# Kernel optimization log

Hardware: AMD Instinct MI355X
Metric: run time of the kernel (lower is better)

## Reference

```python
import jax, jax.numpy as jnp
import numpy as np

N_NODES = 50000


def _gcn_norm(edge_index, num_nodes):
    # PyG gcn_norm with add_self_loops=True, edge_weight=1
    loops = jnp.arange(num_nodes, dtype=edge_index.dtype)
    src = jnp.concatenate([edge_index[0], loops])
    dst = jnp.concatenate([edge_index[1], loops])
    deg = jax.ops.segment_sum(jnp.ones_like(dst, dtype=jnp.float32), dst,
                              num_segments=num_nodes)
    deg_inv_sqrt = jnp.where(deg > 0, jax.lax.rsqrt(jnp.maximum(deg, 1.0)), 0.0)
    norm = deg_inv_sqrt[src] * deg_inv_sqrt[dst]  # [E + N]
    return src, dst, norm


def _gcn_conv(x, src, dst, norm, W, b, num_nodes):
    h = x @ W                                 # [N, out] dense transform first
    msg = h[src] * norm[:, None]              # gather + scale, [E+N, out]
    out = jax.ops.segment_sum(msg, dst, num_segments=num_nodes)  # scatter-add
    return out + b


def setup_inputs() -> dict:
    key = jax.random.key(0)
    k1, k2, k3, k4, k5 = jax.random.split(key, 5)
    in_ch, out_ch = 128, 64
    hid = 2 * out_ch
    x = jax.random.normal(k1, (N_NODES, in_ch), dtype=jnp.float32)
    edge_index = jax.random.randint(k2, (2, 800000), 0, N_NODES, dtype=jnp.int64)
    # Glorot init like PyG GCNConv
    W1 = jax.random.normal(k3, (in_ch, hid), dtype=jnp.float32) * (1.0 / np.sqrt(in_ch))
    b1 = jnp.zeros((hid,), dtype=jnp.float32)
    W2 = jax.random.normal(k4, (hid, out_ch), dtype=jnp.float32) * (1.0 / np.sqrt(hid))
    b2 = jnp.zeros((out_ch,), dtype=jnp.float32)
    return {"x": x, "edge_index": edge_index, "W1": W1, "b1": b1,
            "W2": W2, "b2": b2}


def reference(x, edge_index, W1, b1, W2, b2):
    num_nodes = x.shape[0]
    src, dst, norm = _gcn_norm(edge_index, num_nodes)
    h = _gcn_conv(x, src, dst, norm, W1, b1, num_nodes)
    h = jax.nn.relu(h)
    return _gcn_conv(h, src, dst, norm, W2, b2, num_nodes)
```

## Files before the change

### kernel.cpp

```cpp
#include <hip/hip_runtime.h>

#define N_NODES 50000
#define N_EDGES 800000
#define IN_CH   128
#define HID     128
#define OUT_CH  64

#define NBUCK 196
#define BCAP  5120
#define XPAD  136

#define G1_BLOCKS ((N_NODES + 63) / 64)
#define GSPLIT 391

typedef __attribute__((ext_vector_type(8))) short bf16x8;
typedef __attribute__((ext_vector_type(4))) float f32x4;
typedef unsigned short ushort_t;

__device__ __forceinline__ unsigned short f2bf(float f) {
    unsigned u = __float_as_uint(f);
    u += 0x7fffu + ((u >> 16) & 1u);
    return (unsigned short)(u >> 16);
}
__device__ __forceinline__ unsigned pack2(float a, float b) {
    return (unsigned)f2bf(a) | ((unsigned)f2bf(b) << 16);
}
__device__ __forceinline__ float bf_lo(unsigned u) { return __uint_as_float(u << 16); }
__device__ __forceinline__ float bf_hi(unsigned u) { return __uint_as_float(u & 0xffff0000u); }


__global__ __launch_bounds__(256) void k_prep(const float* __restrict__ W1,
                                              const float* __restrict__ W2,
                                              ushort_t* __restrict__ W1t,
                                              ushort_t* __restrict__ W2t,
                                              int* __restrict__ bcur) {
    if (blockIdx.x == 0 && threadIdx.x < NBUCK) bcur[threadIdx.x] = 0;
    int i = blockIdx.x * 256 + threadIdx.x;
    if (i < 128 * 128) {
        int k = i >> 7, c = i & 127;
        W1t[c * 128 + k] = f2bf(W1[k * 128 + c]);
    } else {
        int j = i - 128 * 128;
        if (j < 128 * 64) {
            int k = j >> 6, c = j & 63;
            W2t[c * 128 + k] = f2bf(W2[k * 64 + c]);
        }
    }
}


__global__ __launch_bounds__(256) void k_stage(const int phase, const int tile0,
                                               const int* __restrict__ src,
                                               const int* __restrict__ dst,
                                               int* __restrict__ bcur,
                                               unsigned* __restrict__ rec,
                                               const float* __restrict__ x,
                                               const ushort_t* __restrict__ W1t,
                                               ushort_t* __restrict__ g,
                                               int* __restrict__ row_beg,
                                               int* __restrict__ row_end,
                                               float* __restrict__ dis,
                                               int* __restrict__ col) {
    __shared__ char smem[52224];
    const int tid = threadIdx.x;

    if (blockIdx.x < NBUCK) {
        if (phase == 0) {
            int* cnt  = (int*)smem;
            int* boff = cnt + 256;
            int* gdel = boff + 256;
            int* bid  = gdel + 256;
            unsigned* stage = (unsigned*)(bid + 4096);

            const int base = blockIdx.x * 4096;
            const int nval = min(4096, N_EDGES - base);

            int dreg[16];
#pragma unroll
            for (int k = 0; k < 16; ++k) {
                int e = base + k * 256 + tid;
                dreg[k] = (e < N_EDGES) ? dst[e] : -1;
            }
            cnt[tid] = 0;
            __syncthreads();
#pragma unroll
            for (int k = 0; k < 16; ++k)
                if (dreg[k] >= 0) atomicAdd(&cnt[dreg[k] >> 8], 1);
            __syncthreads();
            int* s = bid;
            int c = cnt[tid];
            s[tid] = c;
            __syncthreads();
            for (int off = 1; off < 256; off <<= 1) {
                int u = (tid >= off) ? s[tid - off] : 0;
                __syncthreads();
                s[tid] += u;
                __syncthreads();
            }
            boff[tid] = s[tid] - c;
            if (tid < NBUCK && c > 0)
                gdel[tid] = tid * BCAP + atomicAdd(&bcur[tid], c) - boff[tid];
            __syncthreads();
            cnt[tid] = 0;
            __syncthreads();
#pragma unroll
            for (int k = 0; k < 16; ++k) {
                int e = base + k * 256 + tid;
                if (dreg[k] >= 0) {
                    int b = dreg[k] >> 8;
                    int rk = atomicAdd(&cnt[b], 1);
                    int p = boff[b] + rk;
                    stage[p] = (unsigned)src[e] | ((unsigned)(dreg[k] & 255) << 16);
                    bid[p] = b;
                }
            }
            __syncthreads();
            for (int i = tid; i < nval; i += 256) {
                int b = bid[i];
                int p = i + gdel[b];
                if (p < (b + 1) * BCAP)
                    rec[p] = stage[i];
            }
        } else {
            int* hist = (int*)smem;
            int* sbuf = hist + 256;
            int* cur  = sbuf + 256;
            unsigned* stage = (unsigned*)(cur + 256);
            const int b = blockIdx.x;
            const int lo = b * BCAP;
            const int cnt = min(bcur[b], BCAP);

            hist[tid] = 0;
            __syncthreads();
            for (int j = tid; j < cnt; j += 256)
                atomicAdd(&hist[rec[lo + j] >> 16], 1);
            __syncthreads();
            int deg = hist[tid];
            sbuf[tid] = deg;
            __syncthreads();
            for (int off = 1; off < 256; off <<= 1) {
                int u = (tid >= off) ? sbuf[tid - off] : 0;
                __syncthreads();
                sbuf[tid] += u;
                __syncthreads();
            }
            int lbeg = sbuf[tid] - deg;
            int node = (b << 8) + tid;
            if (node < N_NODES) {
                row_beg[node] = lo + lbeg;
                row_end[node] = lo + lbeg + deg;
                dis[node] = rsqrtf((float)deg + 1.0f);
            }
            cur[tid] = lbeg;
            __syncthreads();
            for (int j = tid; j < cnt; j += 256) {
                unsigned r = rec[lo + j];
                int rk = atomicAdd(&cur[r >> 16], 1);
                stage[rk] = r & 0xffffu;
            }
            __syncthreads();
            for (int i = tid; i < cnt; i += 256)
                col[lo + i] = (int)stage[i];
        }
    } else {
        ushort_t* xs = (ushort_t*)smem;
        ushort_t* ws = (ushort_t*)(smem + 17408);
        const int bid = tile0 + (blockIdx.x - NBUCK);
        const int row0 = bid * 64;

        for (int i = tid; i < 64 * 32; i += 256) {
            int r = i >> 5, k4 = (i & 31) << 2;
            int gr = row0 + r;
            float4 v = make_float4(0.f, 0.f, 0.f, 0.f);
            if (gr < N_NODES) v = *(const float4*)&x[(long)gr * IN_CH + k4];
            ushort4 u;
            u.x = f2bf(v.x); u.y = f2bf(v.y); u.z = f2bf(v.z); u.w = f2bf(v.w);
            *(ushort4*)&xs[r * XPAD + k4] = u;
        }
        for (int i = tid; i < 128 * 16; i += 256) {
            int c = i >> 4, seg = i & 15;
            *(uint4*)&ws[c * XPAD + seg * 8] = *(const uint4*)&W1t[c * 128 + seg * 8];
        }
        __syncthreads();

        const int w = tid >> 6, lane = tid & 63;
        const int m = lane & 15, q = lane >> 4;
        const ushort_t* arow = &xs[(w * 16 + m) * XPAD + q * 8];
        const ushort_t* brow = &ws[m * XPAD + q * 8];

        f32x4 acc[8] = {};
#pragma unroll
        for (int k0 = 0; k0 < 128; k0 += 32) {
            bf16x8 a = *(const bf16x8*)(arow + k0);
#pragma unroll
            for (int nt = 0; nt < 8; ++nt) {
                bf16x8 b = *(const bf16x8*)(brow + nt * 16 * XPAD + k0);
                acc[nt] = __builtin_amdgcn_mfma_f32_16x16x32_bf16(a, b, acc[nt], 0, 0, 0);
            }
        }

#pragma unroll
        for (int reg = 0; reg < 4; ++reg) {
            int gr = row0 + w * 16 + q * 4 + reg;
            if (gr < N_NODES) {
#pragma unroll
                for (int nt = 0; nt < 8; ++nt)
                    g[(long)gr * HID + nt * 16 + m] = f2bf(acc[nt][reg]);
            }
        }
    }
}


__global__ __launch_bounds__(256) void k_agg1g2(const int* __restrict__ row_beg,
                                                const int* __restrict__ row_end,
                                                const int* __restrict__ col,
                                                const float* __restrict__ dis,
                                                const ushort_t* __restrict__ g1,
                                                const float* __restrict__ b1,
                                                const ushort_t* __restrict__ W2t,
                                                ushort_t* __restrict__ g3) {
    __shared__ ushort_t hs[16 * XPAD];
    const int tid = threadIdx.x;
    const int w = tid >> 6, lane = tid & 63;
    const int q = lane >> 4;
    const int seg = lane & 15;
    const int cl = seg << 3;
    const uint4* G = (const uint4*)g1;
    const int r0 = blockIdx.x * 16;

    for (int rr = 0; rr < 4; ++rr) {
        const int r = r0 + w * 4 + rr;
        const int beg = row_beg[r], end = row_end[r];

        float acc[8] = {};
        int e = beg + q;
        for (; e + 4 < end; e += 8) {
            int s0 = col[e], s1 = col[e + 4];
            float d0 = dis[s0], d1 = dis[s1];
            uint4 u0 = G[(long)s0 * 16 + seg];
            uint4 u1 = G[(long)s1 * 16 + seg];
            acc[0] += bf_lo(u0.x) * d0; acc[1] += bf_hi(u0.x) * d0;
            acc[2] += bf_lo(u0.y) * d0; acc[3] += bf_hi(u0.y) * d0;
            acc[4] += bf_lo(u0.z) * d0; acc[5] += bf_hi(u0.z) * d0;
            acc[6] += bf_lo(u0.w) * d0; acc[7] += bf_hi(u0.w) * d0;
            acc[0] += bf_lo(u1.x) * d1; acc[1] += bf_hi(u1.x) * d1;
            acc[2] += bf_lo(u1.y) * d1; acc[3] += bf_hi(u1.y) * d1;
            acc[4] += bf_lo(u1.z) * d1; acc[5] += bf_hi(u1.z) * d1;
            acc[6] += bf_lo(u1.w) * d1; acc[7] += bf_hi(u1.w) * d1;
        }
        if (e < end) {
            int s0 = col[e];
            float d0 = dis[s0];
            uint4 u = G[(long)s0 * 16 + seg];
            acc[0] += bf_lo(u.x) * d0; acc[1] += bf_hi(u.x) * d0;
            acc[2] += bf_lo(u.y) * d0; acc[3] += bf_hi(u.y) * d0;
            acc[4] += bf_lo(u.z) * d0; acc[5] += bf_hi(u.z) * d0;
            acc[6] += bf_lo(u.w) * d0; acc[7] += bf_hi(u.w) * d0;
        }
#pragma unroll
        for (int off = 16; off < 64; off <<= 1)
#pragma unroll
            for (int j = 0; j < 8; ++j) acc[j] += __shfl_xor(acc[j], off);

        if (q == 0) {
            const float d = dis[r];
            uint4 u = G[(long)r * 16 + seg];
            acc[0] += bf_lo(u.x) * d; acc[1] += bf_hi(u.x) * d;
            acc[2] += bf_lo(u.y) * d; acc[3] += bf_hi(u.y) * d;
            acc[4] += bf_lo(u.z) * d; acc[5] += bf_hi(u.z) * d;
            acc[6] += bf_lo(u.w) * d; acc[7] += bf_hi(u.w) * d;
            float o[8];
#pragma unroll
            for (int j = 0; j < 8; ++j) o[j] = fmaxf(acc[j] * d + b1[cl + j], 0.f);
            uint4 pw;
            pw.x = pack2(o[0], o[1]); pw.y = pack2(o[2], o[3]);
            pw.z = pack2(o[4], o[5]); pw.w = pack2(o[6], o[7]);
            *(uint4*)&hs[(w * 4 + rr) * XPAD + cl] = pw;
        }
    }
    __syncthreads();

    const int m = lane & 15;
    const ushort_t* arow = &hs[m * XPAD + q * 8];
    const ushort_t* brow = &W2t[(w * 16 + m) * 128 + q * 8];

    f32x4 acc2 = {};
#pragma unroll
    for (int k0 = 0; k0 < 128; k0 += 32) {
        bf16x8 a = *(const bf16x8*)(arow + k0);
        bf16x8 b = *(const bf16x8*)(brow + k0);
        acc2 = __builtin_amdgcn_mfma_f32_16x16x32_bf16(a, b, acc2, 0, 0, 0);
    }

#pragma unroll
    for (int reg = 0; reg < 4; ++reg) {
        int gr = r0 + q * 4 + reg;
        float d = dis[gr];
        g3[(long)gr * OUT_CH + w * 16 + m] = f2bf(acc2[reg] * d);
    }
}


__global__ __launch_bounds__(256) void k_agg2(const int* __restrict__ row_beg,
                                              const int* __restrict__ row_end,
                                              const int* __restrict__ col,
                                              const float* __restrict__ dis,
                                              const ushort_t* __restrict__ g3,
                                              const float* __restrict__ b2,
                                              float* __restrict__ out) {
    int r = blockIdx.x * 4 + (threadIdx.x >> 6);
    if (r >= N_NODES) return;
    const int lane = threadIdx.x & 63;
    const int q = lane >> 3;
    const int seg = lane & 7;
    const int cl = seg << 3;
    const uint4* G = (const uint4*)g3;
    const int beg = row_beg[r], end = row_end[r];

    float acc[8] = {};
    int e = beg + q;
    for (; e + 8 < end; e += 16) {
        int s0 = col[e], s1 = col[e + 8];
        uint4 u0 = G[(long)s0 * 8 + seg];
        uint4 u1 = G[(long)s1 * 8 + seg];
        acc[0] += bf_lo(u0.x); acc[1] += bf_hi(u0.x);
        acc[2] += bf_lo(u0.y); acc[3] += bf_hi(u0.y);
        acc[4] += bf_lo(u0.z); acc[5] += bf_hi(u0.z);
        acc[6] += bf_lo(u0.w); acc[7] += bf_hi(u0.w);
        acc[0] += bf_lo(u1.x); acc[1] += bf_hi(u1.x);
        acc[2] += bf_lo(u1.y); acc[3] += bf_hi(u1.y);
        acc[4] += bf_lo(u1.z); acc[5] += bf_hi(u1.z);
        acc[6] += bf_lo(u1.w); acc[7] += bf_hi(u1.w);
    }
    if (e < end) {
        int s = col[e];
        uint4 u = G[(long)s * 8 + seg];
        acc[0] += bf_lo(u.x); acc[1] += bf_hi(u.x);
        acc[2] += bf_lo(u.y); acc[3] += bf_hi(u.y);
        acc[4] += bf_lo(u.z); acc[5] += bf_hi(u.z);
        acc[6] += bf_lo(u.w); acc[7] += bf_hi(u.w);
    }
#pragma unroll
    for (int off = 8; off < 64; off <<= 1)
#pragma unroll
        for (int j = 0; j < 8; ++j) acc[j] += __shfl_xor(acc[j], off);

    if (q == 0) {
        uint4 u = G[(long)r * 8 + seg];
        acc[0] += bf_lo(u.x); acc[1] += bf_hi(u.x);
        acc[2] += bf_lo(u.y); acc[3] += bf_hi(u.y);
        acc[4] += bf_lo(u.z); acc[5] += bf_hi(u.z);
        acc[6] += bf_lo(u.w); acc[7] += bf_hi(u.w);
        const float d = dis[r];
        float4 o0, o1;
        o0.x = acc[0] * d + b2[cl + 0];
        o0.y = acc[1] * d + b2[cl + 1];
        o0.z = acc[2] * d + b2[cl + 2];
        o0.w = acc[3] * d + b2[cl + 3];
        o1.x = acc[4] * d + b2[cl + 4];
        o1.y = acc[5] * d + b2[cl + 5];
        o1.z = acc[6] * d + b2[cl + 6];
        o1.w = acc[7] * d + b2[cl + 7];
        *(float4*)&out[(long)r * OUT_CH + cl] = o0;
        *(float4*)&out[(long)r * OUT_CH + cl + 4] = o1;
    }
}


extern "C" void kernel_launch(void* const* d_in, const int* in_sizes, int n_in,
                              void* d_out, int out_size, void* d_ws, size_t ws_size,
                              hipStream_t stream) {
    const float* x   = (const float*)d_in[0];
    const int*   ei  = (const int*)d_in[1];
    const float* W1  = (const float*)d_in[2];
    const float* b1  = (const float*)d_in[3];
    const float* W2  = (const float*)d_in[4];
    const float* b2  = (const float*)d_in[5];
    float* out = (float*)d_out;

    const int* src = ei;
    const int* dst = ei + N_EDGES;

    char* p = (char*)d_ws;
    unsigned* rec = (unsigned*)p;         p += (long)NBUCK * BCAP * 4;
    int* col     = (int*)p;               p += (long)NBUCK * BCAP * 4;
    int* row_beg = (int*)p;               p += 50048 * 4;
    int* row_end = (int*)p;               p += 50048 * 4;
    int* bcur    = (int*)p;               p += 256 * 4;
    float* dis   = (float*)p;             p += 50048 * 4;
    ushort_t* W1t = (ushort_t*)p;         p += 128 * 128 * 2;
    ushort_t* W2t = (ushort_t*)p;         p += 128 * 64 * 2;
    ushort_t* g1  = (ushort_t*)p;         p += (long)N_NODES * HID * 2;
    ushort_t* g3  = (ushort_t*)p;

    const int B = 256;

    k_prep<<<96, B, 0, stream>>>(W1, W2, W1t, W2t, bcur);
    k_stage<<<NBUCK + GSPLIT, B, 0, stream>>>(0, 0, src, dst, bcur, rec,
                                              x, W1t, g1, row_beg, row_end, dis, col);
    k_stage<<<NBUCK + (G1_BLOCKS - GSPLIT), B, 0, stream>>>(1, GSPLIT, src, dst, bcur, rec,
                                              x, W1t, g1, row_beg, row_end, dis, col);
    k_agg1g2<<<3125, B, 0, stream>>>(row_beg, row_end, col, dis, g1, b1, W2t, g3);
    k_agg2<<<(N_NODES + 3) / 4, B, 0, stream>>>(row_beg, row_end, col, dis, g3, b2, out);
}
```

Measured before the change: 173.0 us.

## Drop global CSR build; rebuild per-bucket CSR in shared memory inside aggregation kernels

Removes the phase-1 CSR pass that wrote col/row_beg/row_end to global memory. A small k_dis kernel now computes degrees, and each aggregation block re-sorts its 256-node bucket's edge records into shared memory before gathering. All GEMM tiles for g1 now run in a single launch alongside bucketing. This saves global writes and reads of the column index arrays and one launch, but every block repeats the bucket histogram, scan and scatter 16 times per bucket in both aggregation kernels.

```diff
diff --git a/kernel.cpp b/kernel.cpp
--- a/kernel.cpp
+++ b/kernel.cpp
@@ -11,7 +11,6 @@
 #define XPAD  136
 
 #define G1_BLOCKS ((N_NODES + 63) / 64)
-#define GSPLIT 391
 
 typedef __attribute__((ext_vector_type(8))) short bf16x8;
 typedef __attribute__((ext_vector_type(4))) float f32x4;
@@ -49,123 +48,76 @@
 }
 
 
-__global__ __launch_bounds__(256) void k_stage(const int phase, const int tile0,
-                                               const int* __restrict__ src,
-                                               const int* __restrict__ dst,
-                                               int* __restrict__ bcur,
-                                               unsigned* __restrict__ rec,
-                                               const float* __restrict__ x,
-                                               const ushort_t* __restrict__ W1t,
-                                               ushort_t* __restrict__ g,
-                                               int* __restrict__ row_beg,
-                                               int* __restrict__ row_end,
-                                               float* __restrict__ dis,
-                                               int* __restrict__ col) {
+__global__ __launch_bounds__(256) void k_stage0(const int* __restrict__ src,
+                                                const int* __restrict__ dst,
+                                                int* __restrict__ bcur,
+                                                unsigned* __restrict__ rec,
+                                                const float* __restrict__ x,
+                                                const ushort_t* __restrict__ W1t,
+                                                ushort_t* __restrict__ g1) {
     __shared__ char smem[52224];
     const int tid = threadIdx.x;
 
     if (blockIdx.x < NBUCK) {
-        if (phase == 0) {
-            int* cnt  = (int*)smem;
-            int* boff = cnt + 256;
-            int* gdel = boff + 256;
-            int* bid  = gdel + 256;
-            unsigned* stage = (unsigned*)(bid + 4096);
-
-            const int base = blockIdx.x * 4096;
-            const int nval = min(4096, N_EDGES - base);
-
-            int dreg[16];
-#pragma unroll
-            for (int k = 0; k < 16; ++k) {
-                int e = base + k * 256 + tid;
-                dreg[k] = (e < N_EDGES) ? dst[e] : -1;
+        int* cnt  = (int*)smem;
+        int* boff = cnt + 256;
+        int* gdel = boff + 256;
+        int* bid  = gdel + 256;
+        unsigned* stage = (unsigned*)(bid + 4096);
+
+        const int base = blockIdx.x * 4096;
+        const int nval = min(4096, N_EDGES - base);
+
+        int dreg[16];
+#pragma unroll
+        for (int k = 0; k < 16; ++k) {
+            int e = base + k * 256 + tid;
+            dreg[k] = (e < N_EDGES) ? dst[e] : -1;
+        }
+        cnt[tid] = 0;
+        __syncthreads();
+#pragma unroll
+        for (int k = 0; k < 16; ++k)
+            if (dreg[k] >= 0) atomicAdd(&cnt[dreg[k] >> 8], 1);
+        __syncthreads();
+        int* s = bid;
+        int c = cnt[tid];
+        s[tid] = c;
+        __syncthreads();
+        for (int off = 1; off < 256; off <<= 1) {
+            int u = (tid >= off) ? s[tid - off] : 0;
+            __syncthreads();
+            s[tid] += u;
+            __syncthreads();
+        }
+        boff[tid] = s[tid] - c;
+        if (tid < NBUCK && c > 0)
+            gdel[tid] = tid * BCAP + atomicAdd(&bcur[tid], c) - boff[tid];
+        __syncthreads();
+        cnt[tid] = 0;
+        __syncthreads();
+#pragma unroll
+        for (int k = 0; k < 16; ++k) {
+            int e = base + k * 256 + tid;
+            if (dreg[k] >= 0) {
+                int b = dreg[k] >> 8;
+                int rk = atomicAdd(&cnt[b], 1);
+                int p = boff[b] + rk;
+                stage[p] = (unsigned)src[e] | ((unsigned)(dreg[k] & 255) << 16);
+                bid[p] = b;
             }
-            cnt[tid] = 0;
-            __syncthreads();
-#pragma unroll
-            for (int k = 0; k < 16; ++k)
-                if (dreg[k] >= 0) atomicAdd(&cnt[dreg[k] >> 8], 1);
-            __syncthreads();
-            int* s = bid;
-            int c = cnt[tid];
-            s[tid] = c;
-            __syncthreads();
-            for (int off = 1; off < 256; off <<= 1) {
-                int u = (tid >= off) ? s[tid - off] : 0;
-                __syncthreads();
-                s[tid] += u;
-                __syncthreads();
-            }
-            boff[tid] = s[tid] - c;
-            if (tid < NBUCK && c > 0)
-                gdel[tid] = tid * BCAP + atomicAdd(&bcur[tid], c) - boff[tid];
-            __syncthreads();
-            cnt[tid] = 0;
-            __syncthreads();
-#pragma unroll
-            for (int k = 0; k < 16; ++k) {
-                int e = base + k * 256 + tid;
-                if (dreg[k] >= 0) {
-                    int b = dreg[k] >> 8;
-                    int rk = atomicAdd(&cnt[b], 1);
-                    int p = boff[b] + rk;
-                    stage[p] = (unsigned)src[e] | ((unsigned)(dreg[k] & 255) << 16);
-                    bid[p] = b;
-                }
-            }
-            __syncthreads();
-            for (int i = tid; i < nval; i += 256) {
-                int b = bid[i];
-                int p = i + gdel[b];
-                if (p < (b + 1) * BCAP)
-                    rec[p] = stage[i];
-            }
-        } else {
-            int* hist = (int*)smem;
-            int* sbuf = hist + 256;
-            int* cur  = sbuf + 256;
-            unsigned* stage = (unsigned*)(cur + 256);
-            const int b = blockIdx.x;
-            const int lo = b * BCAP;
-            const int cnt = min(bcur[b], BCAP);
-
-            hist[tid] = 0;
-            __syncthreads();
-            for (int j = tid; j < cnt; j += 256)
-                atomicAdd(&hist[rec[lo + j] >> 16], 1);
-            __syncthreads();
-            int deg = hist[tid];
-            sbuf[tid] = deg;
-            __syncthreads();
-            for (int off = 1; off < 256; off <<= 1) {
-                int u = (tid >= off) ? sbuf[tid - off] : 0;
-                __syncthreads();
-                sbuf[tid] += u;
-                __syncthreads();
-            }
-            int lbeg = sbuf[tid] - deg;
-            int node = (b << 8) + tid;
-            if (node < N_NODES) {
-                row_beg[node] = lo + lbeg;
-                row_end[node] = lo + lbeg + deg;
-                dis[node] = rsqrtf((float)deg + 1.0f);
-            }
-            cur[tid] = lbeg;
-            __syncthreads();
-            for (int j = tid; j < cnt; j += 256) {
-                unsigned r = rec[lo + j];
-                int rk = atomicAdd(&cur[r >> 16], 1);
-                stage[rk] = r & 0xffffu;
-            }
-            __syncthreads();
-            for (int i = tid; i < cnt; i += 256)
-                col[lo + i] = (int)stage[i];
+        }
+        __syncthreads();
+        for (int i = tid; i < nval; i += 256) {
+            int b = bid[i];
+            int p = i + gdel[b];
+            if (p < (b + 1) * BCAP)
+                rec[p] = stage[i];
         }
     } else {
         ushort_t* xs = (ushort_t*)smem;
         ushort_t* ws = (ushort_t*)(smem + 17408);
-        const int bid = tile0 + (blockIdx.x - NBUCK);
+        const int bid = blockIdx.x - NBUCK;
         const int row0 = bid * 64;
 
         for (int i = tid; i < 64 * 32; i += 256) {
@@ -205,38 +157,89 @@
             if (gr < N_NODES) {
 #pragma unroll
                 for (int nt = 0; nt < 8; ++nt)
-                    g[(long)gr * HID + nt * 16 + m] = f2bf(acc[nt][reg]);
+                    g1[(long)gr * HID + nt * 16 + m] = f2bf(acc[nt][reg]);
             }
         }
     }
 }
 
 
-__global__ __launch_bounds__(256) void k_agg1g2(const int* __restrict__ row_beg,
-                                                const int* __restrict__ row_end,
-                                                const int* __restrict__ col,
-                                                const float* __restrict__ dis,
-                                                const ushort_t* __restrict__ g1,
-                                                const float* __restrict__ b1,
-                                                const ushort_t* __restrict__ W2t,
-                                                ushort_t* __restrict__ g3) {
+__global__ __launch_bounds__(256) void k_dis(const int* __restrict__ bcur,
+                                             const unsigned* __restrict__ rec,
+                                             float* __restrict__ dis) {
+    __shared__ int hist[256];
+    const int tid = threadIdx.x;
+    const int b = blockIdx.x;
+    const int lo = b * BCAP;
+    const int cnt = min(bcur[b], BCAP);
+    hist[tid] = 0;
+    __syncthreads();
+    for (int j = tid; j < cnt; j += 256)
+        atomicAdd(&hist[rec[lo + j] >> 16], 1);
+    __syncthreads();
+    int node = (b << 8) + tid;
+    if (node < N_NODES) dis[node] = rsqrtf((float)hist[tid] + 1.0f);
+}
+
+
+__global__ __launch_bounds__(256) void k_agg1x(const int* __restrict__ bcur,
+                                               const unsigned* __restrict__ rec,
+                                               const float* __restrict__ dis,
+                                               const ushort_t* __restrict__ g1,
+                                               const float* __restrict__ b1,
+                                               const ushort_t* __restrict__ W2t,
+                                               ushort_t* __restrict__ g3) {
+    __shared__ int deg_s[256];
+    __shared__ int beg_s[256];
+    __shared__ int cur_s[256];
+    __shared__ float disl[256];
+    __shared__ int stage_src[BCAP];
     __shared__ ushort_t hs[16 * XPAD];
     const int tid = threadIdx.x;
+    const int b = blockIdx.x >> 4, sl = blockIdx.x & 15;
+    const int lo = b * BCAP;
+    const int cntb = min(bcur[b], BCAP);
+
+    deg_s[tid] = 0;
+    __syncthreads();
+    for (int j = tid; j < cntb; j += 256)
+        atomicAdd(&deg_s[rec[lo + j] >> 16], 1);
+    __syncthreads();
+    int dg = deg_s[tid];
+    cur_s[tid] = dg;
+    __syncthreads();
+    for (int off = 1; off < 256; off <<= 1) {
+        int u = (tid >= off) ? cur_s[tid - off] : 0;
+        __syncthreads();
+        cur_s[tid] += u;
+        __syncthreads();
+    }
+    beg_s[tid] = cur_s[tid] - dg;
+    disl[tid] = rsqrtf((float)dg + 1.0f);
+    cur_s[tid] = beg_s[tid];
+    __syncthreads();
+    for (int j = tid; j < cntb; j += 256) {
+        unsigned r = rec[lo + j];
+        int rk = atomicAdd(&cur_s[r >> 16], 1);
+        stage_src[rk] = (int)(r & 0xffffu);
+    }
+    __syncthreads();
+
     const int w = tid >> 6, lane = tid & 63;
     const int q = lane >> 4;
     const int seg = lane & 15;
     const int cl = seg << 3;
     const uint4* G = (const uint4*)g1;
-    const int r0 = blockIdx.x * 16;
 
     for (int rr = 0; rr < 4; ++rr) {
-        const int r = r0 + w * 4 + rr;
-        const int beg = row_beg[r], end = row_end[r];
+        const int t = sl * 16 + w * 4 + rr;
+        const int r = (b << 8) + t;
+        const int beg = beg_s[t], end = beg + deg_s[t];
 
         float acc[8] = {};
         int e = beg + q;
         for (; e + 4 < end; e += 8) {
-            int s0 = col[e], s1 = col[e + 4];
+            int s0 = stage_src[e], s1 = stage_src[e + 4];
             float d0 = dis[s0], d1 = dis[s1];
             uint4 u0 = G[(long)s0 * 16 + seg];
             uint4 u1 = G[(long)s1 * 16 + seg];
@@ -250,7 +253,7 @@
             acc[6] += bf_lo(u1.w) * d1; acc[7] += bf_hi(u1.w) * d1;
         }
         if (e < end) {
-            int s0 = col[e];
+            int s0 = stage_src[e];
             float d0 = dis[s0];
             uint4 u = G[(long)s0 * 16 + seg];
             acc[0] += bf_lo(u.x) * d0; acc[1] += bf_hi(u.x) * d0;
@@ -264,19 +267,25 @@
             for (int j = 0; j < 8; ++j) acc[j] += __shfl_xor(acc[j], off);
 
         if (q == 0) {
-            const float d = dis[r];
-            uint4 u = G[(long)r * 16 + seg];
-            acc[0] += bf_lo(u.x) * d; acc[1] += bf_hi(u.x) * d;
-            acc[2] += bf_lo(u.y) * d; acc[3] += bf_hi(u.y) * d;
-            acc[4] += bf_lo(u.z) * d; acc[5] += bf_hi(u.z) * d;
-            acc[6] += bf_lo(u.w) * d; acc[7] += bf_hi(u.w) * d;
-            float o[8];
-#pragma unroll
-            for (int j = 0; j < 8; ++j) o[j] = fmaxf(acc[j] * d + b1[cl + j], 0.f);
-            uint4 pw;
-            pw.x = pack2(o[0], o[1]); pw.y = pack2(o[2], o[3]);
-            pw.z = pack2(o[4], o[5]); pw.w = pack2(o[6], o[7]);
-            *(uint4*)&hs[(w * 4 + rr) * XPAD + cl] = pw;
+            const int hrow = w * 4 + rr;
+            if (r < N_NODES) {
+                const float d = disl[t];
+                uint4 u = G[(long)r * 16 + seg];
+                acc[0] += bf_lo(u.x) * d; acc[1] += bf_hi(u.x) * d;
+                acc[2] += bf_lo(u.y) * d; acc[3] += bf_hi(u.y) * d;
+                acc[4] += bf_lo(u.z) * d; acc[5] += bf_hi(u.z) * d;
+                acc[6] += bf_lo(u.w) * d; acc[7] += bf_hi(u.w) * d;
+                float o[8];
+#pragma unroll
+                for (int j = 0; j < 8; ++j) o[j] = fmaxf(acc[j] * d + b1[cl + j], 0.f);
+                uint4 pw;
+                pw.x = pack2(o[0], o[1]); pw.y = pack2(o[2], o[3]);
+                pw.z = pack2(o[4], o[5]); pw.w = pack2(o[6], o[7]);
+                *(uint4*)&hs[hrow * XPAD + cl] = pw;
+            } else {
+                uint4 z = make_uint4(0u, 0u, 0u, 0u);
+                *(uint4*)&hs[hrow * XPAD + cl] = z;
+            }
         }
     }
     __syncthreads();
@@ -295,75 +304,114 @@
 
 #pragma unroll
     for (int reg = 0; reg < 4; ++reg) {
-        int gr = r0 + q * 4 + reg;
-        float d = dis[gr];
-        g3[(long)gr * OUT_CH + w * 16 + m] = f2bf(acc2[reg] * d);
-    }
-}
-
-
-__global__ __launch_bounds__(256) void k_agg2(const int* __restrict__ row_beg,
-                                              const int* __restrict__ row_end,
-                                              const int* __restrict__ col,
-                                              const float* __restrict__ dis,
-                                              const ushort_t* __restrict__ g3,
-                                              const float* __restrict__ b2,
-                                              float* __restrict__ out) {
-    int r = blockIdx.x * 4 + (threadIdx.x >> 6);
-    if (r >= N_NODES) return;
-    const int lane = threadIdx.x & 63;
+        const int t = sl * 16 + q * 4 + reg;
+        const int gr = (b << 8) + t;
+        if (gr < N_NODES) {
+            float d = disl[t];
+            g3[(long)gr * OUT_CH + w * 16 + m] = f2bf(acc2[reg] * d);
+        }
+    }
+}
+
+
+__global__ __launch_bounds__(256) void k_agg2x(const int* __restrict__ bcur,
+                                               const unsigned* __restrict__ rec,
+                                               const ushort_t* __restrict__ g3,
+                                               const float* __restrict__ b2,
+                                               float* __restrict__ out) {
+    __shared__ int deg_s[256];
+    __shared__ int beg_s[256];
+    __shared__ int cur_s[256];
+    __shared__ float disl[256];
+    __shared__ int stage_src[BCAP];
+    const int tid = threadIdx.x;
+    const int b = blockIdx.x >> 4, sl = blockIdx.x & 15;
+    const int lo = b * BCAP;
+    const int cntb = min(bcur[b], BCAP);
+
+    deg_s[tid] = 0;
+    __syncthreads();
+    for (int j = tid; j < cntb; j += 256)
+        atomicAdd(&deg_s[rec[lo + j] >> 16], 1);
+    __syncthreads();
+    int dg = deg_s[tid];
+    cur_s[tid] = dg;
+    __syncthreads();
+    for (int off = 1; off < 256; off <<= 1) {
+        int u = (tid >= off) ? cur_s[tid - off] : 0;
+        __syncthreads();
+        cur_s[tid] += u;
+        __syncthreads();
+    }
+    beg_s[tid] = cur_s[tid] - dg;
+    disl[tid] = rsqrtf((float)dg + 1.0f);
+    cur_s[tid] = beg_s[tid];
+    __syncthreads();
+    for (int j = tid; j < cntb; j += 256) {
+        unsigned r = rec[lo + j];
+        int rk = atomicAdd(&cur_s[r >> 16], 1);
+        stage_src[rk] = (int)(r & 0xffffu);
+    }
+    __syncthreads();
+
+    const int w = tid >> 6, lane = tid & 63;
     const int q = lane >> 3;
     const int seg = lane & 7;
     const int cl = seg << 3;
     const uint4* G = (const uint4*)g3;
-    const int beg = row_beg[r], end = row_end[r];
-
-    float acc[8] = {};
-    int e = beg + q;
-    for (; e + 8 < end; e += 16) {
-        int s0 = col[e], s1 = col[e + 8];
-        uint4 u0 = G[(long)s0 * 8 + seg];
-        uint4 u1 = G[(long)s1 * 8 + seg];
-        acc[0] += bf_lo(u0.x); acc[1] += bf_hi(u0.x);
-        acc[2] += bf_lo(u0.y); acc[3] += bf_hi(u0.y);
-        acc[4] += bf_lo(u0.z); acc[5] += bf_hi(u0.z);
-        acc[6] += bf_lo(u0.w); acc[7] += bf_hi(u0.w);
-        acc[0] += bf_lo(u1.x); acc[1] += bf_hi(u1.x);
-        acc[2] += bf_lo(u1.y); acc[3] += bf_hi(u1.y);
-        acc[4] += bf_lo(u1.z); acc[5] += bf_hi(u1.z);
-        acc[6] += bf_lo(u1.w); acc[7] += bf_hi(u1.w);
-    }
-    if (e < end) {
-        int s = col[e];
-        uint4 u = G[(long)s * 8 + seg];
-        acc[0] += bf_lo(u.x); acc[1] += bf_hi(u.x);
-        acc[2] += bf_lo(u.y); acc[3] += bf_hi(u.y);
-        acc[4] += bf_lo(u.z); acc[5] += bf_hi(u.z);
-        acc[6] += bf_lo(u.w); acc[7] += bf_hi(u.w);
-    }
-#pragma unroll
-    for (int off = 8; off < 64; off <<= 1)
-#pragma unroll
-        for (int j = 0; j < 8; ++j) acc[j] += __shfl_xor(acc[j], off);
-
-    if (q == 0) {
-        uint4 u = G[(long)r * 8 + seg];
-        acc[0] += bf_lo(u.x); acc[1] += bf_hi(u.x);
-        acc[2] += bf_lo(u.y); acc[3] += bf_hi(u.y);
-        acc[4] += bf_lo(u.z); acc[5] += bf_hi(u.z);
-        acc[6] += bf_lo(u.w); acc[7] += bf_hi(u.w);
-        const float d = dis[r];
-        float4 o0, o1;
-        o0.x = acc[0] * d + b2[cl + 0];
-        o0.y = acc[1] * d + b2[cl + 1];
-        o0.z = acc[2] * d + b2[cl + 2];
-        o0.w = acc[3] * d + b2[cl + 3];
-        o1.x = acc[4] * d + b2[cl + 4];
-        o1.y = acc[5] * d + b2[cl + 5];
-        o1.z = acc[6] * d + b2[cl + 6];
-        o1.w = acc[7] * d + b2[cl + 7];
-        *(float4*)&out[(long)r * OUT_CH + cl] = o0;
-        *(float4*)&out[(long)r * OUT_CH + cl + 4] = o1;
+
+    for (int rr = 0; rr < 4; ++rr) {
+        const int t = sl * 16 + w * 4 + rr;
+        const int r = (b << 8) + t;
+        const int beg = beg_s[t], end = beg + deg_s[t];
+
+        float acc[8] = {};
+        int e = beg + q;
+        for (; e + 8 < end; e += 16) {
+            int s0 = stage_src[e], s1 = stage_src[e + 8];
+            uint4 u0 = G[(long)s0 * 8 + seg];
+            uint4 u1 = G[(long)s1 * 8 + seg];
+            acc[0] += bf_lo(u0.x); acc[1] += bf_hi(u0.x);
+            acc[2] += bf_lo(u0.y); acc[3] += bf_hi(u0.y);
+            acc[4] += bf_lo(u0.z); acc[5] += bf_hi(u0.z);
+            acc[6] += bf_lo(u0.w); acc[7] += bf_hi(u0.w);
+            acc[0] += bf_lo(u1.x); acc[1] += bf_hi(u1.x);
+            acc[2] += bf_lo(u1.y); acc[3] += bf_hi(u1.y);
+            acc[4] += bf_lo(u1.z); acc[5] += bf_hi(u1.z);
+            acc[6] += bf_lo(u1.w); acc[7] += bf_hi(u1.w);
+        }
+        if (e < end) {
+            int s = stage_src[e];
+            uint4 u = G[(long)s * 8 + seg];
+            acc[0] += bf_lo(u.x); acc[1] += bf_hi(u.x);
+            acc[2] += bf_lo(u.y); acc[3] += bf_hi(u.y);
+            acc[4] += bf_lo(u.z); acc[5] += bf_hi(u.z);
+            acc[6] += bf_lo(u.w); acc[7] += bf_hi(u.w);
+        }
+#pragma unroll
+        for (int off = 8; off < 64; off <<= 1)
+#pragma unroll
+            for (int j = 0; j < 8; ++j) acc[j] += __shfl_xor(acc[j], off);
+
+        if (q == 0 && r < N_NODES) {
+            uint4 u = G[(long)r * 8 + seg];
+            acc[0] += bf_lo(u.x); acc[1] += bf_hi(u.x);
+            acc[2] += bf_lo(u.y); acc[3] += bf_hi(u.y);
+            acc[4] += bf_lo(u.z); acc[5] += bf_hi(u.z);
+            acc[6] += bf_lo(u.w); acc[7] += bf_hi(u.w);
+            const float d = disl[t];
+            float4 o0, o1;
+            o0.x = acc[0] * d + b2[cl + 0];
+            o0.y = acc[1] * d + b2[cl + 1];
+            o0.z = acc[2] * d + b2[cl + 2];
+            o0.w = acc[3] * d + b2[cl + 3];
+            o1.x = acc[4] * d + b2[cl + 4];
+            o1.y = acc[5] * d + b2[cl + 5];
+            o1.z = acc[6] * d + b2[cl + 6];
+            o1.w = acc[7] * d + b2[cl + 7];
+            *(float4*)&out[(long)r * OUT_CH + cl] = o0;
+            *(float4*)&out[(long)r * OUT_CH + cl + 4] = o1;
+        }
     }
 }
 
@@ -384,9 +432,6 @@
 
     char* p = (char*)d_ws;
     unsigned* rec = (unsigned*)p;         p += (long)NBUCK * BCAP * 4;
-    int* col     = (int*)p;               p += (long)NBUCK * BCAP * 4;
-    int* row_beg = (int*)p;               p += 50048 * 4;
-    int* row_end = (int*)p;               p += 50048 * 4;
     int* bcur    = (int*)p;               p += 256 * 4;
     float* dis   = (float*)p;             p += 50048 * 4;
     ushort_t* W1t = (ushort_t*)p;         p += 128 * 128 * 2;
@@ -394,13 +439,9 @@
     ushort_t* g1  = (ushort_t*)p;         p += (long)N_NODES * HID * 2;
     ushort_t* g3  = (ushort_t*)p;
 
-    const int B = 256;
-
-    k_prep<<<96, B, 0, stream>>>(W1, W2, W1t, W2t, bcur);
-    k_stage<<<NBUCK + GSPLIT, B, 0, stream>>>(0, 0, src, dst, bcur, rec,
-                                              x, W1t, g1, row_beg, row_end, dis, col);
-    k_stage<<<NBUCK + (G1_BLOCKS - GSPLIT), B, 0, stream>>>(1, GSPLIT, src, dst, bcur, rec,
-                                              x, W1t, g1, row_beg, row_end, dis, col);
-    k_agg1g2<<<3125, B, 0, stream>>>(row_beg, row_end, col, dis, g1, b1, W2t, g3);
-    k_agg2<<<(N_NODES + 3) / 4, B, 0, stream>>>(row_beg, row_end, col, dis, g3, b2, out);
-}
+    k_prep<<<96, 256, 0, stream>>>(W1, W2, W1t, W2t, bcur);
+    k_stage0<<<NBUCK + G1_BLOCKS, 256, 0, stream>>>(src, dst, bcur, rec, x, W1t, g1);
+    k_dis<<<NBUCK, 256, 0, stream>>>(bcur, rec, dis);
+    k_agg1x<<<NBUCK * 16, 256, 0, stream>>>(bcur, rec, dis, g1, b1, W2t, g3);
+    k_agg2x<<<NBUCK * 16, 256, 0, stream>>>(bcur, rec, g3, b2, out);
+}
```

Result: slower. 210.7 us (+21.8%).

## Move all GEMM1 tiles into bucket-scatter launch and split CSR build per half-bucket

Applied to the files above, without the earlier changes.

All first-layer GEMM tiles now launch with the phase-0 bucket scatter, instead of half of them riding along with the CSR-build phase. CSR construction becomes its own kernel with two blocks per bucket. Each block rebuilds the histogram but scatters only the half of the nodes it owns, which doubles parallelism for the CSR step and uses a smaller static LDS footprint. The cost is a redundant histogram pass per bucket, and the CSR phase no longer overlaps with GEMM work.

```diff
diff --git a/kernel.cpp b/kernel.cpp
--- a/kernel.cpp
+++ b/kernel.cpp
@@ -11,7 +11,6 @@
 #define XPAD  136
 
 #define G1_BLOCKS ((N_NODES + 63) / 64)
-#define GSPLIT 391
 
 typedef __attribute__((ext_vector_type(8))) short bf16x8;
 typedef __attribute__((ext_vector_type(4))) float f32x4;
@@ -49,123 +48,76 @@
 }
 
 
-__global__ __launch_bounds__(256) void k_stage(const int phase, const int tile0,
-                                               const int* __restrict__ src,
-                                               const int* __restrict__ dst,
-                                               int* __restrict__ bcur,
-                                               unsigned* __restrict__ rec,
-                                               const float* __restrict__ x,
-                                               const ushort_t* __restrict__ W1t,
-                                               ushort_t* __restrict__ g,
-                                               int* __restrict__ row_beg,
-                                               int* __restrict__ row_end,
-                                               float* __restrict__ dis,
-                                               int* __restrict__ col) {
+__global__ __launch_bounds__(256) void k_stage0(const int* __restrict__ src,
+                                                const int* __restrict__ dst,
+                                                int* __restrict__ bcur,
+                                                unsigned* __restrict__ rec,
+                                                const float* __restrict__ x,
+                                                const ushort_t* __restrict__ W1t,
+                                                ushort_t* __restrict__ g1) {
     __shared__ char smem[52224];
     const int tid = threadIdx.x;
 
     if (blockIdx.x < NBUCK) {
-        if (phase == 0) {
-            int* cnt  = (int*)smem;
-            int* boff = cnt + 256;
-            int* gdel = boff + 256;
-            int* bid  = gdel + 256;
-            unsigned* stage = (unsigned*)(bid + 4096);
-
-            const int base = blockIdx.x * 4096;
-            const int nval = min(4096, N_EDGES - base);
-
-            int dreg[16];
-#pragma unroll
-            for (int k = 0; k < 16; ++k) {
-                int e = base + k * 256 + tid;
-                dreg[k] = (e < N_EDGES) ? dst[e] : -1;
+        int* cnt  = (int*)smem;
+        int* boff = cnt + 256;
+        int* gdel = boff + 256;
+        int* bid  = gdel + 256;
+        unsigned* stage = (unsigned*)(bid + 4096);
+
+        const int base = blockIdx.x * 4096;
+        const int nval = min(4096, N_EDGES - base);
+
+        int dreg[16];
+#pragma unroll
+        for (int k = 0; k < 16; ++k) {
+            int e = base + k * 256 + tid;
+            dreg[k] = (e < N_EDGES) ? dst[e] : -1;
+        }
+        cnt[tid] = 0;
+        __syncthreads();
+#pragma unroll
+        for (int k = 0; k < 16; ++k)
+            if (dreg[k] >= 0) atomicAdd(&cnt[dreg[k] >> 8], 1);
+        __syncthreads();
+        int* s = bid;
+        int c = cnt[tid];
+        s[tid] = c;
+        __syncthreads();
+        for (int off = 1; off < 256; off <<= 1) {
+            int u = (tid >= off) ? s[tid - off] : 0;
+            __syncthreads();
+            s[tid] += u;
+            __syncthreads();
+        }
+        boff[tid] = s[tid] - c;
+        if (tid < NBUCK && c > 0)
+            gdel[tid] = tid * BCAP + atomicAdd(&bcur[tid], c) - boff[tid];
+        __syncthreads();
+        cnt[tid] = 0;
+        __syncthreads();
+#pragma unroll
+        for (int k = 0; k < 16; ++k) {
+            int e = base + k * 256 + tid;
+            if (dreg[k] >= 0) {
+                int b = dreg[k] >> 8;
+                int rk = atomicAdd(&cnt[b], 1);
+                int p = boff[b] + rk;
+                stage[p] = (unsigned)src[e] | ((unsigned)(dreg[k] & 255) << 16);
+                bid[p] = b;
             }
-            cnt[tid] = 0;
-            __syncthreads();
-#pragma unroll
-            for (int k = 0; k < 16; ++k)
-                if (dreg[k] >= 0) atomicAdd(&cnt[dreg[k] >> 8], 1);
-            __syncthreads();
-            int* s = bid;
-            int c = cnt[tid];
-            s[tid] = c;
-            __syncthreads();
-            for (int off = 1; off < 256; off <<= 1) {
-                int u = (tid >= off) ? s[tid - off] : 0;
-                __syncthreads();
-                s[tid] += u;
-                __syncthreads();
-            }
-            boff[tid] = s[tid] - c;
-            if (tid < NBUCK && c > 0)
-                gdel[tid] = tid * BCAP + atomicAdd(&bcur[tid], c) - boff[tid];
-            __syncthreads();
-            cnt[tid] = 0;
-            __syncthreads();
-#pragma unroll
-            for (int k = 0; k < 16; ++k) {
-                int e = base + k * 256 + tid;
-                if (dreg[k] >= 0) {
-                    int b = dreg[k] >> 8;
-                    int rk = atomicAdd(&cnt[b], 1);
-                    int p = boff[b] + rk;
-                    stage[p] = (unsigned)src[e] | ((unsigned)(dreg[k] & 255) << 16);
-                    bid[p] = b;
-                }
-            }
-            __syncthreads();
-            for (int i = tid; i < nval; i += 256) {
-                int b = bid[i];
-                int p = i + gdel[b];
-                if (p < (b + 1) * BCAP)
-                    rec[p] = stage[i];
-            }
-        } else {
-            int* hist = (int*)smem;
-            int* sbuf = hist + 256;
-            int* cur  = sbuf + 256;
-            unsigned* stage = (unsigned*)(cur + 256);
-            const int b = blockIdx.x;
-            const int lo = b * BCAP;
-            const int cnt = min(bcur[b], BCAP);
-
-            hist[tid] = 0;
-            __syncthreads();
-            for (int j = tid; j < cnt; j += 256)
-                atomicAdd(&hist[rec[lo + j] >> 16], 1);
-            __syncthreads();
-            int deg = hist[tid];
-            sbuf[tid] = deg;
-            __syncthreads();
-            for (int off = 1; off < 256; off <<= 1) {
-                int u = (tid >= off) ? sbuf[tid - off] : 0;
-                __syncthreads();
-                sbuf[tid] += u;
-                __syncthreads();
-            }
-            int lbeg = sbuf[tid] - deg;
-            int node = (b << 8) + tid;
-            if (node < N_NODES) {
-                row_beg[node] = lo + lbeg;
-                row_end[node] = lo + lbeg + deg;
-                dis[node] = rsqrtf((float)deg + 1.0f);
-            }
-            cur[tid] = lbeg;
-            __syncthreads();
-            for (int j = tid; j < cnt; j += 256) {
-                unsigned r = rec[lo + j];
-                int rk = atomicAdd(&cur[r >> 16], 1);
-                stage[rk] = r & 0xffffu;
-            }
-            __syncthreads();
-            for (int i = tid; i < cnt; i += 256)
-                col[lo + i] = (int)stage[i];
+        }
+        __syncthreads();
+        for (int i = tid; i < nval; i += 256) {
+            int b = bid[i];
+            int p = i + gdel[b];
+            if (p < (b + 1) * BCAP)
+                rec[p] = stage[i];
         }
     } else {
         ushort_t* xs = (ushort_t*)smem;
         ushort_t* ws = (ushort_t*)(smem + 17408);
-        const int bid = tile0 + (blockIdx.x - NBUCK);
+        const int bid = blockIdx.x - NBUCK;
         const int row0 = bid * 64;
 
         for (int i = tid; i < 64 * 32; i += 256) {
@@ -205,10 +157,65 @@
             if (gr < N_NODES) {
 #pragma unroll
                 for (int nt = 0; nt < 8; ++nt)
-                    g[(long)gr * HID + nt * 16 + m] = f2bf(acc[nt][reg]);
+                    g1[(long)gr * HID + nt * 16 + m] = f2bf(acc[nt][reg]);
             }
         }
     }
+}
+
+
+__global__ __launch_bounds__(256) void k_csr2(const int* __restrict__ bcur,
+                                              const unsigned* __restrict__ rec,
+                                              int* __restrict__ row_beg,
+                                              int* __restrict__ row_end,
+                                              float* __restrict__ dis,
+                                              int* __restrict__ col) {
+    __shared__ int hist[256];
+    __shared__ int sbuf[256];
+    __shared__ int cur[256];
+    __shared__ unsigned stage[BCAP];
+    const int tid = threadIdx.x;
+    const int b = blockIdx.x >> 1, hf = blockIdx.x & 1;
+    const int lo = b * BCAP;
+    const int cnt = min(bcur[b], BCAP);
+
+    hist[tid] = 0;
+    __syncthreads();
+    for (int j = tid; j < cnt; j += 256)
+        atomicAdd(&hist[rec[lo + j] >> 16], 1);
+    __syncthreads();
+    int deg = hist[tid];
+    sbuf[tid] = deg;
+    __syncthreads();
+    for (int off = 1; off < 256; off <<= 1) {
+        int u = (tid >= off) ? sbuf[tid - off] : 0;
+        __syncthreads();
+        sbuf[tid] += u;
+        __syncthreads();
+    }
+    int lbeg = sbuf[tid] - deg;
+    const int node = (b << 8) + tid;
+    if ((tid >> 7) == hf && node < N_NODES) {
+        row_beg[node] = lo + lbeg;
+        row_end[node] = lo + lbeg + deg;
+        dis[node] = rsqrtf((float)deg + 1.0f);
+    }
+    cur[tid] = lbeg;
+    __syncthreads();
+    const int seg0 = hf ? sbuf[127] : 0;
+    const int seg1 = hf ? cnt : sbuf[127];
+    __syncthreads();
+    for (int j = tid; j < cnt; j += 256) {
+        unsigned r = rec[lo + j];
+        int n = (int)(r >> 16);
+        if ((n >> 7) == hf) {
+            int rk = atomicAdd(&cur[n], 1);
+            stage[rk - seg0] = r & 0xffffu;
+        }
+    }
+    __syncthreads();
+    for (int i = seg0 + tid; i < seg1; i += 256)
+        col[lo + i] = (int)stage[i - seg0];
 }
 
 
@@ -394,13 +401,9 @@
     ushort_t* g1  = (ushort_t*)p;         p += (long)N_NODES * HID * 2;
     ushort_t* g3  = (ushort_t*)p;
 
-    const int B = 256;
-
-    k_prep<<<96, B, 0, stream>>>(W1, W2, W1t, W2t, bcur);
-    k_stage<<<NBUCK + GSPLIT, B, 0, stream>>>(0, 0, src, dst, bcur, rec,
-                                              x, W1t, g1, row_beg, row_end, dis, col);
-    k_stage<<<NBUCK + (G1_BLOCKS - GSPLIT), B, 0, stream>>>(1, GSPLIT, src, dst, bcur, rec,
-                                              x, W1t, g1, row_beg, row_end, dis, col);
-    k_agg1g2<<<3125, B, 0, stream>>>(row_beg, row_end, col, dis, g1, b1, W2t, g3);
-    k_agg2<<<(N_NODES + 3) / 4, B, 0, stream>>>(row_beg, row_end, col, dis, g3, b2, out);
-}
+    k_prep<<<96, 256, 0, stream>>>(W1, W2, W1t, W2t, bcur);
+    k_stage0<<<NBUCK + G1_BLOCKS, 256, 0, stream>>>(src, dst, bcur, rec, x, W1t, g1);
+    k_csr2<<<NBUCK * 2, 256, 0, stream>>>(bcur, rec, row_beg, row_end, dis, col);
+    k_agg1g2<<<3125, 256, 0, stream>>>(row_beg, row_end, col, dis, g1, b1, W2t, g3);
+    k_agg2<<<(N_NODES + 3) / 4, 256, 0, stream>>>(row_beg, row_end, col, dis, g3, b2, out);
+}
```

Result: no change. 174.6 us (+1.0%).
